# Kernel optimization log

Hardware: AMD Instinct MI355X
Metric: run time of the kernel (lower is better)

Reference implementation:

```python
import jax, jax.numpy as jnp
import numpy as np

B, T, F = 1024, 512, 64
H1, H2, D1, D2, NOUT = 32, 16, 16, 8, 1


def setup_inputs() -> dict:
    key = jax.random.key(0)
    ks = jax.random.split(key, 14)
    s = lambda k, shape, fan: jax.random.normal(k, shape, jnp.float32) / np.sqrt(fan)
    return {
        "x": jax.random.normal(ks[0], (B, T, F), jnp.float32),
        "Wx1": s(ks[1], (F, H1), F),
        "Wh1": s(ks[2], (H1, H1), H1),
        "b1": jnp.zeros((H1,), jnp.float32),
        "Wx2": s(ks[3], (H1, H2), H1),
        "Wh2": s(ks[4], (H2, H2), H2),
        "b2": jnp.zeros((H2,), jnp.float32),
        "W3": s(ks[5], (H2, D1), H2),
        "b3": jnp.zeros((D1,), jnp.float32),
        "W4": s(ks[6], (D1, D2), D1),
        "b4": jnp.zeros((D2,), jnp.float32),
        "Wo": s(ks[7], (D2, NOUT), D2),
        "bo": jnp.zeros((NOUT,), jnp.float32),
    }


def reference(x, Wx1, Wh1, b1, Wx2, Wh2, b2, W3, b3, W4, b4, Wo, bo):
    b = x.shape[0]
    # SimpleRNN 1 (return_sequences=True): h_t = tanh(x_t Wx + h_{t-1} Wh + b)
    # Precompute input projection for all timesteps: [T, B, H1]
    xp1 = jnp.swapaxes(jnp.einsum('btf,fh->bth', x, Wx1) + b1, 0, 1)

    def step1(h, xt):
        h = jnp.tanh(xt + h @ Wh1)
        return h, h

    _, seq1 = jax.lax.scan(step1, jnp.zeros((b, Wh1.shape[0]), x.dtype), xp1)
    # SimpleRNN 2 (return_sequences=False): keep only final state
    xp2 = seq1 @ Wx2 + b2  # [T, B, H2]

    def step2(h, xt):
        h = jnp.tanh(xt + h @ Wh2)
        return h, None

    h2, _ = jax.lax.scan(step2, jnp.zeros((b, Wh2.shape[0]), x.dtype), xp2)
    # Dense head
    y = jax.nn.relu(h2 @ W3 + b3)
    y = y @ W4 + b4
    return y @ Wo + bo
```

## Files before the change

kernel.cpp:

```cpp
#include <hip/hip_runtime.h>

#define BB 1024
#define TB 512
#define FB 64
#define NH1 32
#define NH2 16
#define ND1 16
#define ND2 8

#define WAVE_FENCE() __builtin_amdgcn_fence(__ATOMIC_ACQ_REL, "wavefront")

__device__ __forceinline__ float tanh_fast(float v) {
    float e = __expf(2.0f * v);
    return fmaf(-2.0f, __builtin_amdgcn_rcpf(e + 1.0f), 1.0f);
}

__global__ __attribute__((amdgpu_flat_work_group_size(64, 64)))
           __attribute__((amdgpu_waves_per_eu(1, 1)))
void rnn_fused_kernel(
    const float* __restrict__ x,
    const float* __restrict__ Wx1, const float* __restrict__ Wh1, const float* __restrict__ b1,
    const float* __restrict__ Wx2, const float* __restrict__ Wh2, const float* __restrict__ b2,
    const float* __restrict__ W3,  const float* __restrict__ b3,
    const float* __restrict__ W4,  const float* __restrict__ b4,
    const float* __restrict__ Wo,  const float* __restrict__ bo,
    float* __restrict__ out)
{
    __shared__ __align__(16) float xs[2][FB];
    __shared__ __align__(16) float h1s[NH1];
    __shared__ __align__(16) float h2s[NH2];
    __shared__ __align__(16) float ys[ND1];

    const int lane = threadIdx.x;
    const int h = lane & 31;
    const int p = lane >> 5;
    const int g = lane & 15;
    const int q = lane >> 4;
    const int b = blockIdx.x;

    auto w1 = [&](int i) { return Wx1[(32 * p + i) * NH1 + h]; };
    auto r1 = [&](int i) { return Wh1[(16 * p + i) * NH1 + h]; };
    auto w2 = [&](int i) { return Wx2[(8 * q + i) * NH2 + g]; };
    auto r2 = [&](int i) { return Wh2[(4 * q + i) * NH2 + g]; };
    const float4 wxa = make_float4(w1(0),  w1(1),  w1(2),  w1(3));
    const float4 wxb = make_float4(w1(4),  w1(5),  w1(6),  w1(7));
    const float4 wxc = make_float4(w1(8),  w1(9),  w1(10), w1(11));
    const float4 wxd = make_float4(w1(12), w1(13), w1(14), w1(15));
    const float4 wxe = make_float4(w1(16), w1(17), w1(18), w1(19));
    const float4 wxf = make_float4(w1(20), w1(21), w1(22), w1(23));
    const float4 wxg = make_float4(w1(24), w1(25), w1(26), w1(27));
    const float4 wxh = make_float4(w1(28), w1(29), w1(30), w1(31));
    const float4 wha = make_float4(r1(0),  r1(1),  r1(2),  r1(3));
    const float4 whb = make_float4(r1(4),  r1(5),  r1(6),  r1(7));
    const float4 whc = make_float4(r1(8),  r1(9),  r1(10), r1(11));
    const float4 whd = make_float4(r1(12), r1(13), r1(14), r1(15));
    const float4 x2a = make_float4(w2(0), w2(1), w2(2), w2(3));
    const float4 x2b = make_float4(w2(4), w2(5), w2(6), w2(7));
    const float4 h2w = make_float4(r2(0), r2(1), r2(2), r2(3));
    const float b1v = (p == 0) ? b1[h] : 0.0f;
    const float b2v = (q == 0) ? b2[g] : 0.0f;

    if (lane < NH1) h1s[lane] = 0.0f;
    if (lane < NH2) h2s[lane] = 0.0f;

    const float* xb = x + (size_t)b * TB * FB + lane;
    float xq0 = xb[0 * FB];
    float xq1 = xb[1 * FB];
    float xq2 = xb[2 * FB];
    float xq3 = xb[3 * FB];
    xs[0][lane] = xq0;
    __syncthreads();

#define STEP(T, SLOT, QSTAGE, QREFILL)                                         \
    {                                                                          \
        WAVE_FENCE();            \
        const int t_ = (T);                                                    \
        int tn_ = t_ + 4; tn_ = (tn_ < TB) ? tn_ : (TB - 1);                   \
        const float xnew_ = xb[tn_ * FB];                                      \
        xs[(SLOT) ^ 1][lane] = QSTAGE;                                         \
        float4 hva = *(const float4*)&h1s[16 * p + 0];                         \
        float4 hvb = *(const float4*)&h1s[16 * p + 4];                         \
        float4 hvc = *(const float4*)&h1s[16 * p + 8];                         \
        float4 hvd = *(const float4*)&h1s[16 * p + 12];                        \
        const float4* xv = (const float4*)&xs[SLOT][32 * p];                   \
        float a0 = b1v, a1 = 0.0f, a2 = 0.0f, a3 = 0.0f;                       \
        float4 v_;                                                             \
        v_ = xv[0]; a0 = fmaf(v_.x, wxa.x, a0); a1 = fmaf(v_.y, wxa.y, a1);    \
                    a2 = fmaf(v_.z, wxa.z, a2); a3 = fmaf(v_.w, wxa.w, a3);    \
        v_ = xv[1]; a0 = fmaf(v_.x, wxb.x, a0); a1 = fmaf(v_.y, wxb.y, a1);    \
                    a2 = fmaf(v_.z, wxb.z, a2); a3 = fmaf(v_.w, wxb.w, a3);    \
        v_ = xv[2]; a0 = fmaf(v_.x, wxc.x, a0); a1 = fmaf(v_.y, wxc.y, a1);    \
                    a2 = fmaf(v_.z, wxc.z, a2); a3 = fmaf(v_.w, wxc.w, a3);    \
        v_ = xv[3]; a0 = fmaf(v_.x, wxd.x, a0); a1 = fmaf(v_.y, wxd.y, a1);    \
                    a2 = fmaf(v_.z, wxd.z, a2); a3 = fmaf(v_.w, wxd.w, a3);    \
        v_ = xv[4]; a0 = fmaf(v_.x, wxe.x, a0); a1 = fmaf(v_.y, wxe.y, a1);    \
                    a2 = fmaf(v_.z, wxe.z, a2); a3 = fmaf(v_.w, wxe.w, a3);    \
        v_ = xv[5]; a0 = fmaf(v_.x, wxf.x, a0); a1 = fmaf(v_.y, wxf.y, a1);    \
                    a2 = fmaf(v_.z, wxf.z, a2); a3 = fmaf(v_.w, wxf.w, a3);    \
        v_ = xv[6]; a0 = fmaf(v_.x, wxg.x, a0); a1 = fmaf(v_.y, wxg.y, a1);    \
                    a2 = fmaf(v_.z, wxg.z, a2); a3 = fmaf(v_.w, wxg.w, a3);    \
        v_ = xv[7]; a0 = fmaf(v_.x, wxh.x, a0); a1 = fmaf(v_.y, wxh.y, a1);    \
                    a2 = fmaf(v_.z, wxh.z, a2); a3 = fmaf(v_.w, wxh.w, a3);    \
        a0 = fmaf(hva.x, wha.x, a0); a1 = fmaf(hva.y, wha.y, a1);              \
        a2 = fmaf(hva.z, wha.z, a2); a3 = fmaf(hva.w, wha.w, a3);              \
        a0 = fmaf(hvb.x, whb.x, a0); a1 = fmaf(hvb.y, whb.y, a1);              \
        a2 = fmaf(hvb.z, whb.z, a2); a3 = fmaf(hvb.w, whb.w, a3);              \
        a0 = fmaf(hvc.x, whc.x, a0); a1 = fmaf(hvc.y, whc.y, a1);              \
        a2 = fmaf(hvc.z, whc.z, a2); a3 = fmaf(hvc.w, whc.w, a3);              \
        a0 = fmaf(hvd.x, whd.x, a0); a1 = fmaf(hvd.y, whd.y, a1);              \
        a2 = fmaf(hvd.z, whd.z, a2); a3 = fmaf(hvd.w, whd.w, a3);              \
        float acc = (a0 + a1) + (a2 + a3);                                     \
        acc += __shfl_xor(acc, 32, 64);                                        \
        float h1new = tanh_fast(acc);                                          \
        if (t_ > 0) {    \
            float4 u0 = *(const float4*)&h1s[8 * q + 0];                       \
            float4 u1 = *(const float4*)&h1s[8 * q + 4];                       \
            float4 hw = *(const float4*)&h2s[4 * q];                           \
            float c0 = b2v, c1 = 0.0f;                                         \
            c0 = fmaf(u0.x, x2a.x, c0); c1 = fmaf(u0.y, x2a.y, c1);            \
            c0 = fmaf(u0.z, x2a.z, c0); c1 = fmaf(u0.w, x2a.w, c1);            \
            c0 = fmaf(u1.x, x2b.x, c0); c1 = fmaf(u1.y, x2b.y, c1);            \
            c0 = fmaf(u1.z, x2b.z, c0); c1 = fmaf(u1.w, x2b.w, c1);            \
            c0 = fmaf(hw.x, h2w.x, c0); c1 = fmaf(hw.y, h2w.y, c1);            \
            c0 = fmaf(hw.z, h2w.z, c0); c1 = fmaf(hw.w, h2w.w, c1);            \
            float cc = c0 + c1;                                                \
            cc += __shfl_xor(cc, 16, 64);                                      \
            cc += __shfl_xor(cc, 32, 64);                                      \
            float h2new = tanh_fast(cc);                                       \
            if (lane < NH2) h2s[lane] = h2new;                                 \
        }                                                                      \
        WAVE_FENCE();       \
        if (p == 0) h1s[h] = h1new;                                            \
        QREFILL = xnew_;                                                       \
    }

    for (int tb = 0; tb < TB; tb += 4) {
        STEP(tb + 0, 0, xq1, xq0);
        STEP(tb + 1, 1, xq2, xq1);
        STEP(tb + 2, 0, xq3, xq2);
        STEP(tb + 3, 1, xq0, xq3);
    }
#undef STEP

    WAVE_FENCE();

    {
        float4 u0 = *(const float4*)&h1s[8 * q + 0];
        float4 u1 = *(const float4*)&h1s[8 * q + 4];
        float4 hw = *(const float4*)&h2s[4 * q];
        float c0 = b2v, c1 = 0.0f;
        c0 = fmaf(u0.x, x2a.x, c0); c1 = fmaf(u0.y, x2a.y, c1);
        c0 = fmaf(u0.z, x2a.z, c0); c1 = fmaf(u0.w, x2a.w, c1);
        c0 = fmaf(u1.x, x2b.x, c0); c1 = fmaf(u1.y, x2b.y, c1);
        c0 = fmaf(u1.z, x2b.z, c0); c1 = fmaf(u1.w, x2b.w, c1);
        c0 = fmaf(hw.x, h2w.x, c0); c1 = fmaf(hw.y, h2w.y, c1);
        c0 = fmaf(hw.z, h2w.z, c0); c1 = fmaf(hw.w, h2w.w, c1);
        float cc = c0 + c1;
        cc += __shfl_xor(cc, 16, 64);
        cc += __shfl_xor(cc, 32, 64);
        float h2fin = tanh_fast(cc);
        WAVE_FENCE();
        if (lane < NH2) h2s[lane] = h2fin;
        WAVE_FENCE();
    }

    float a3h = b3[g];
#pragma unroll
    for (int j = 0; j < 16; ++j) a3h = fmaf(h2s[j], W3[j * ND1 + g], a3h);
    float y1 = fmaxf(a3h, 0.0f);
    WAVE_FENCE();
    if (lane < ND1) ys[lane] = y1;
    WAVE_FENCE();

    const int e = lane & 7;
    float a4 = b4[e];
#pragma unroll
    for (int j = 0; j < 16; ++j) a4 = fmaf(ys[j], W4[j * ND2 + e], a4);

    float yo = a4 * Wo[e];
    yo += __shfl_xor(yo, 1, 64);
    yo += __shfl_xor(yo, 2, 64);
    yo += __shfl_xor(yo, 4, 64);
    if (lane == 0) out[b] = yo + bo[0];
}

extern "C" void kernel_launch(void* const* d_in, const int* in_sizes, int n_in,
                              void* d_out, int out_size, void* d_ws, size_t ws_size,
                              hipStream_t stream) {
    const float* x   = (const float*)d_in[0];
    const float* Wx1 = (const float*)d_in[1];
    const float* Wh1 = (const float*)d_in[2];
    const float* b1  = (const float*)d_in[3];
    const float* Wx2 = (const float*)d_in[4];
    const float* Wh2 = (const float*)d_in[5];
    const float* b2  = (const float*)d_in[6];
    const float* W3  = (const float*)d_in[7];
    const float* b3  = (const float*)d_in[8];
    const float* W4  = (const float*)d_in[9];
    const float* b4  = (const float*)d_in[10];
    const float* Wo  = (const float*)d_in[11];
    const float* bo  = (const float*)d_in[12];
    float* out = (float*)d_out;

    rnn_fused_kernel<<<dim3(BB), dim3(64), 0, stream>>>(
        x, Wx1, Wh1, b1, Wx2, Wh2, b2, W3, b3, W4, b4, Wo, bo, out);
}
```

Before: 363.5 us.

## Interleave two batch rows per wavefront to overlap independent recurrence chains

Each 64-lane block now runs two independent batch rows (A and B) through the RNN in lockstep, with separate shared buffers for each. The grid is halved to match. The goal is to hide the latency of the serial per-step chain (LDS loads, shuffles, tanh) by giving the scheduler a second independent dependency chain inside one wave. The layer-2 operands are also loaded up front and the new h1 is stored earlier in each step. The trade-off is that half as many waves are launched, which may leave SIMDs idle, and each wave needs more registers.

```diff
diff --git a/kernel.cpp b/kernel.cpp
--- a/kernel.cpp
+++ b/kernel.cpp
@@ -26,17 +26,18 @@
     const float* __restrict__ Wo,  const float* __restrict__ bo,
     float* __restrict__ out)
 {
-    __shared__ __align__(16) float xs[2][FB];
-    __shared__ __align__(16) float h1s[NH1];
-    __shared__ __align__(16) float h2s[NH2];
-    __shared__ __align__(16) float ys[ND1];
+    __shared__ __align__(16) float xsA[2][FB], xsB[2][FB];
+    __shared__ __align__(16) float h1A[NH1],  h1B[NH1];
+    __shared__ __align__(16) float h2A[NH2],  h2B[NH2];
+    __shared__ __align__(16) float ysA[ND1],  ysB[ND1];
 
     const int lane = threadIdx.x;
     const int h = lane & 31;
     const int p = lane >> 5;
     const int g = lane & 15;
     const int q = lane >> 4;
-    const int b = blockIdx.x;
+    const int bA = blockIdx.x * 2;
+    const int bB = bA + 1;
 
     auto w1 = [&](int i) { return Wx1[(32 * p + i) * NH1 + h]; };
     auto r1 = [&](int i) { return Wh1[(16 * p + i) * NH1 + h]; };
@@ -60,29 +61,31 @@
     const float b1v = (p == 0) ? b1[h] : 0.0f;
     const float b2v = (q == 0) ? b2[g] : 0.0f;
 
-    if (lane < NH1) h1s[lane] = 0.0f;
-    if (lane < NH2) h2s[lane] = 0.0f;
-
-    const float* xb = x + (size_t)b * TB * FB + lane;
-    float xq0 = xb[0 * FB];
-    float xq1 = xb[1 * FB];
-    float xq2 = xb[2 * FB];
-    float xq3 = xb[3 * FB];
-    xs[0][lane] = xq0;
+    if (lane < NH1) { h1A[lane] = 0.0f; h1B[lane] = 0.0f; }
+    if (lane < NH2) { h2A[lane] = 0.0f; h2B[lane] = 0.0f; }
+
+    const float* xpA = x + (size_t)bA * TB * FB + lane;
+    const float* xpB = x + (size_t)bB * TB * FB + lane;
+    float qa0 = xpA[0 * FB], qa1 = xpA[1 * FB], qa2 = xpA[2 * FB], qa3 = xpA[3 * FB];
+    float qb0 = xpB[0 * FB], qb1 = xpB[1 * FB], qb2 = xpB[2 * FB], qb3 = xpB[3 * FB];
+    xsA[0][lane] = qa0;
+    xsB[0][lane] = qb0;
     __syncthreads();
 
-#define STEP(T, SLOT, QSTAGE, QREFILL)                                         \
+#define STEP1(T, SLOT, XS, H1S, H2S, XPTR, QSTAGE, QREFILL)                    \
     {                                                                          \
-        WAVE_FENCE();            \
         const int t_ = (T);                                                    \
         int tn_ = t_ + 4; tn_ = (tn_ < TB) ? tn_ : (TB - 1);                   \
-        const float xnew_ = xb[tn_ * FB];                                      \
-        xs[(SLOT) ^ 1][lane] = QSTAGE;                                         \
-        float4 hva = *(const float4*)&h1s[16 * p + 0];                         \
-        float4 hvb = *(const float4*)&h1s[16 * p + 4];                         \
-        float4 hvc = *(const float4*)&h1s[16 * p + 8];                         \
-        float4 hvd = *(const float4*)&h1s[16 * p + 12];                        \
-        const float4* xv = (const float4*)&xs[SLOT][32 * p];                   \
+        const float xnew_ = XPTR[tn_ * FB];                                    \
+        XS[(SLOT) ^ 1][lane] = QSTAGE;                                         \
+        float4 hva = *(const float4*)&H1S[16 * p + 0];                         \
+        float4 hvb = *(const float4*)&H1S[16 * p + 4];                         \
+        float4 hvc = *(const float4*)&H1S[16 * p + 8];                         \
+        float4 hvd = *(const float4*)&H1S[16 * p + 12];                        \
+        float4 u0 = *(const float4*)&H1S[8 * q + 0];      \
+        float4 u1 = *(const float4*)&H1S[8 * q + 4];                           \
+        float4 hw = *(const float4*)&H2S[4 * q];          \
+        const float4* xv = (const float4*)&XS[SLOT][32 * p];                   \
         float a0 = b1v, a1 = 0.0f, a2 = 0.0f, a3 = 0.0f;                       \
         float4 v_;                                                             \
         v_ = xv[0]; a0 = fmaf(v_.x, wxa.x, a0); a1 = fmaf(v_.y, wxa.y, a1);    \
@@ -112,10 +115,9 @@
         float acc = (a0 + a1) + (a2 + a3);                                     \
         acc += __shfl_xor(acc, 32, 64);                                        \
         float h1new = tanh_fast(acc);                                          \
-        if (t_ > 0) {    \
-            float4 u0 = *(const float4*)&h1s[8 * q + 0];                       \
-            float4 u1 = *(const float4*)&h1s[8 * q + 4];                       \
-            float4 hw = *(const float4*)&h2s[4 * q];                           \
+        WAVE_FENCE();             \
+        if (p == 0) H1S[h] = h1new;      \
+        if (t_ > 0) {                  \
             float c0 = b2v, c1 = 0.0f;                                         \
             c0 = fmaf(u0.x, x2a.x, c0); c1 = fmaf(u0.y, x2a.y, c1);            \
             c0 = fmaf(u0.z, x2a.z, c0); c1 = fmaf(u0.w, x2a.w, c1);            \
@@ -127,61 +129,69 @@
             cc += __shfl_xor(cc, 16, 64);                                      \
             cc += __shfl_xor(cc, 32, 64);                                      \
             float h2new = tanh_fast(cc);                                       \
-            if (lane < NH2) h2s[lane] = h2new;                                 \
+            if (lane < NH2) H2S[lane] = h2new;                                 \
         }                                                                      \
-        WAVE_FENCE();       \
-        if (p == 0) h1s[h] = h1new;                                            \
         QREFILL = xnew_;                                                       \
     }
 
+#define PHASE(T, SLOT, QSA, QRA, QSB, QRB)                                     \
+    {                                                                          \
+        WAVE_FENCE();                 \
+        STEP1(T, SLOT, xsA, h1A, h2A, xpA, QSA, QRA)                           \
+        STEP1(T, SLOT, xsB, h1B, h2B, xpB, QSB, QRB)                           \
+    }
+
     for (int tb = 0; tb < TB; tb += 4) {
-        STEP(tb + 0, 0, xq1, xq0);
-        STEP(tb + 1, 1, xq2, xq1);
-        STEP(tb + 2, 0, xq3, xq2);
-        STEP(tb + 3, 1, xq0, xq3);
-    }
-#undef STEP
+        PHASE(tb + 0, 0, qa1, qa0, qb1, qb0);
+        PHASE(tb + 1, 1, qa2, qa1, qb2, qb1);
+        PHASE(tb + 2, 0, qa3, qa2, qb3, qb2);
+        PHASE(tb + 3, 1, qa0, qa3, qb0, qb3);
+    }
+#undef PHASE
+#undef STEP1
 
     WAVE_FENCE();
 
-    {
-        float4 u0 = *(const float4*)&h1s[8 * q + 0];
-        float4 u1 = *(const float4*)&h1s[8 * q + 4];
-        float4 hw = *(const float4*)&h2s[4 * q];
-        float c0 = b2v, c1 = 0.0f;
-        c0 = fmaf(u0.x, x2a.x, c0); c1 = fmaf(u0.y, x2a.y, c1);
-        c0 = fmaf(u0.z, x2a.z, c0); c1 = fmaf(u0.w, x2a.w, c1);
-        c0 = fmaf(u1.x, x2b.x, c0); c1 = fmaf(u1.y, x2b.y, c1);
-        c0 = fmaf(u1.z, x2b.z, c0); c1 = fmaf(u1.w, x2b.w, c1);
-        c0 = fmaf(hw.x, h2w.x, c0); c1 = fmaf(hw.y, h2w.y, c1);
-        c0 = fmaf(hw.z, h2w.z, c0); c1 = fmaf(hw.w, h2w.w, c1);
-        float cc = c0 + c1;
-        cc += __shfl_xor(cc, 16, 64);
-        cc += __shfl_xor(cc, 32, 64);
-        float h2fin = tanh_fast(cc);
-        WAVE_FENCE();
-        if (lane < NH2) h2s[lane] = h2fin;
-        WAVE_FENCE();
-    }
-
-    float a3h = b3[g];
-#pragma unroll
-    for (int j = 0; j < 16; ++j) a3h = fmaf(h2s[j], W3[j * ND1 + g], a3h);
-    float y1 = fmaxf(a3h, 0.0f);
-    WAVE_FENCE();
-    if (lane < ND1) ys[lane] = y1;
-    WAVE_FENCE();
-
-    const int e = lane & 7;
-    float a4 = b4[e];
-#pragma unroll
-    for (int j = 0; j < 16; ++j) a4 = fmaf(ys[j], W4[j * ND2 + e], a4);
-
-    float yo = a4 * Wo[e];
-    yo += __shfl_xor(yo, 1, 64);
-    yo += __shfl_xor(yo, 2, 64);
-    yo += __shfl_xor(yo, 4, 64);
-    if (lane == 0) out[b] = yo + bo[0];
+#define TAIL(H1S, H2S, YS, BOUT)                                               \
+    {                                                                          \
+        float4 u0 = *(const float4*)&H1S[8 * q + 0];                           \
+        float4 u1 = *(const float4*)&H1S[8 * q + 4];                           \
+        float4 hw = *(const float4*)&H2S[4 * q];                               \
+        float c0 = b2v, c1 = 0.0f;                                             \
+        c0 = fmaf(u0.x, x2a.x, c0); c1 = fmaf(u0.y, x2a.y, c1);                \
+        c0 = fmaf(u0.z, x2a.z, c0); c1 = fmaf(u0.w, x2a.w, c1);                \
+        c0 = fmaf(u1.x, x2b.x, c0); c1 = fmaf(u1.y, x2b.y, c1);                \
+        c0 = fmaf(u1.z, x2b.z, c0); c1 = fmaf(u1.w, x2b.w, c1);                \
+        c0 = fmaf(hw.x, h2w.x, c0); c1 = fmaf(hw.y, h2w.y, c1);                \
+        c0 = fmaf(hw.z, h2w.z, c0); c1 = fmaf(hw.w, h2w.w, c1);                \
+        float cc = c0 + c1;                                                    \
+        cc += __shfl_xor(cc, 16, 64);                                          \
+        cc += __shfl_xor(cc, 32, 64);                                          \
+        float h2fin = tanh_fast(cc);                                           \
+        WAVE_FENCE();                                                          \
+        if (lane < NH2) H2S[lane] = h2fin;                                     \
+        WAVE_FENCE();                                                          \
+        float a3h = b3[g];                                                     \
+        _Pragma("unroll")                                                      \
+        for (int j = 0; j < 16; ++j) a3h = fmaf(H2S[j], W3[j * ND1 + g], a3h); \
+        float y1 = fmaxf(a3h, 0.0f);                                           \
+        WAVE_FENCE();                                                          \
+        if (lane < ND1) YS[lane] = y1;                                         \
+        WAVE_FENCE();                                                          \
+        const int e_ = lane & 7;                                               \
+        float a4 = b4[e_];                                                     \
+        _Pragma("unroll")                                                      \
+        for (int j = 0; j < 16; ++j) a4 = fmaf(YS[j], W4[j * ND2 + e_], a4);   \
+        float yo = a4 * Wo[e_];                                                \
+        yo += __shfl_xor(yo, 1, 64);                                           \
+        yo += __shfl_xor(yo, 2, 64);                                           \
+        yo += __shfl_xor(yo, 4, 64);                                           \
+        if (lane == 0) out[BOUT] = yo + bo[0];                                 \
+    }
+
+    TAIL(h1A, h2A, ysA, bA)
+    TAIL(h1B, h2B, ysB, bB)
+#undef TAIL
 }
 
 extern "C" void kernel_launch(void* const* d_in, const int* in_sizes, int n_in,
@@ -202,6 +212,6 @@
     const float* bo  = (const float*)d_in[12];
     float* out = (float*)d_out;
 
-    rnn_fused_kernel<<<dim3(BB), dim3(64), 0, stream>>>(
+    rnn_fused_kernel<<<dim3(BB / 2), dim3(64), 0, stream>>>(
         x, Wx1, Wh1, b1, Wx2, Wh2, b2, W3, b3, W4, b4, Wo, bo, out);
 }
```

Result: slower. 578.3 us (+59.1%).
